# Optimization experiments

Hardware: AMD Instinct MI355X
Metric: run time of the kernel (lower is better)

The kernel has to match this reference:

```python
import jax, jax.numpy as jnp
import numpy as np

T_STEPS, N, STATE, HID, ACT, C = 32, 64, 64, 128, 32, 96


def setup_inputs() -> dict:
    key = jax.random.key(0)
    ks = jax.random.split(key, 16)
    s = 0.05
    inp = {
        'x': jax.random.normal(ks[0], (T_STEPS, N, STATE), jnp.float32),
        'a': jax.random.normal(ks[1], (T_STEPS, N, ACT), jnp.float32),
        # GRU layer 0 (input state_dim) and layer 1 (input hidden_dim)
        'wih0': jax.random.normal(ks[2], (3 * HID, STATE), jnp.float32) * s,
        'whh0': jax.random.normal(ks[3], (3 * HID, HID), jnp.float32) * s,
        'bih0': jax.random.normal(ks[4], (3 * HID,), jnp.float32) * s,
        'bhh0': jax.random.normal(ks[5], (3 * HID,), jnp.float32) * s,
        'wih1': jax.random.normal(ks[6], (3 * HID, HID), jnp.float32) * s,
        'whh1': jax.random.normal(ks[7], (3 * HID, HID), jnp.float32) * s,
        'bih1': jax.random.normal(ks[8], (3 * HID,), jnp.float32) * s,
        'bhh1': jax.random.normal(ks[9], (3 * HID,), jnp.float32) * s,
        'w1': jax.random.normal(ks[10], (HID, HID + ACT), jnp.float32) * s,
        'b1': jax.random.normal(ks[11], (HID,), jnp.float32) * s,
        'w2': jax.random.normal(ks[12], (1, 2 * HID), jnp.float32) * s,
        'b2': jax.random.normal(ks[13], (1,), jnp.float32) * s,
        'Tm': jax.random.normal(ks[14], (HID, HID, C), jnp.float32),  # init.normal(T,0,1)
    }
    return inp


def _gru_cell(x_t, h, wih, whh, bih, bhh):
    gi = x_t @ wih.T + bih            # (N, 3H)
    gh = h @ whh.T + bhh
    i_r, i_z, i_n = jnp.split(gi, 3, axis=-1)
    h_r, h_z, h_n = jnp.split(gh, 3, axis=-1)
    r = jax.nn.sigmoid(i_r + h_r)
    z = jax.nn.sigmoid(i_z + h_z)
    n = jnp.tanh(i_n + r * h_n)
    return (1.0 - z) * n + z * h


def reference(x, a, wih0, whh0, bih0, bhh0, wih1, whh1, bih1, bhh1, w1, b1, w2, b2, Tm):
    def step(h, x_t):
        h0 = _gru_cell(x_t, h[0], wih0, whh0, bih0, bhh0)
        h1 = _gru_cell(h0, h[1], wih1, whh1, bih1, bhh1)
        return jnp.stack([h0, h1]), h1

    h_init = jnp.zeros((2, N, HID), x.dtype)
    _, p = jax.lax.scan(step, h_init, x)              # (T, N, H)

    fc1 = jax.nn.relu(jnp.concatenate([p, a], -1) @ w1.T + b1)  # (T, N, H)

    Tflat = Tm.reshape(HID, HID * C)

    def batch_discrim(xt):  # xt: (N, H)
        M = (xt @ Tflat).reshape(N, HID, C)           # (N, B, C)
        # pairwise L1 over C: (N, N, B)
        norm = jnp.abs(M[:, None] - M[None, :]).sum(-1)
        o_b = (jnp.exp(-norm).sum(0) - 1.0) / (N - 1)  # (N, B)
        return jnp.concatenate([xt, o_b], 1)          # (N, 2H)

    fc2 = jax.lax.map(batch_discrim, fc1)             # (T, N, 2H)
    prob = jax.nn.sigmoid(fc2 @ w2.T + b2)            # (T, N, 1)
    return prob
```

## Files before the change

kernel.cpp:

```cpp
#include <hip/hip_runtime.h>
#include <hip/hip_fp16.h>
#include <cstdint>

#define T_STEPS 32
#define NB 64
#define STATE 64
#define HID 128
#define ACT 32
#define CDIM 96
#define G3 (3*HID)

typedef __attribute__((ext_vector_type(8))) short short8;
typedef __attribute__((ext_vector_type(4))) float f32x4;
typedef _Float16 h2v __attribute__((ext_vector_type(2)));

__device__ __forceinline__ unsigned short f2bf(float f){
  unsigned int u = __builtin_bit_cast(unsigned int, f);
  u = u + 0x7FFFu + ((u >> 16) & 1u);
  return (unsigned short)(u >> 16);
}
__device__ __forceinline__ float bf2f(unsigned short u){
  unsigned int v = ((unsigned int)u) << 16; return __builtin_bit_cast(float, v);
}
__device__ __forceinline__ unsigned int packh2(float f0, float f1){
  return (unsigned int)__half_as_ushort(__float2half_rn(f0)) |
         ((unsigned int)__half_as_ushort(__float2half_rn(f1)) << 16);
}
__device__ __forceinline__ float sigmoidf_(float x){ return 1.0f/(1.0f + __expf(-x)); }
__device__ __forceinline__ float tanhf_(float x){ float e = __expf(2.0f*x); return (e-1.0f)/(e+1.0f); }

__device__ __forceinline__ float dot2f(float acc, unsigned int a, unsigned int b){
  h2v av = __builtin_bit_cast(h2v, a);
  h2v bv = __builtin_bit_cast(h2v, b);
  return __builtin_amdgcn_fdot2(av, bv, acc, false);
}
__device__ __forceinline__ float l1d(float acc, unsigned int ua, unsigned int ub){
  __half2 a = __builtin_bit_cast(__half2, ua);
  __half2 b = __builtin_bit_cast(__half2, ub);
  __half2 d = __habs2(__hsub2(a, b));
  h2v dv = __builtin_bit_cast(h2v, d);
  h2v ones; ones[0] = (_Float16)1.0f; ones[1] = (_Float16)1.0f;
  return __builtin_amdgcn_fdot2(dv, ones, acc, false);
}
__device__ __forceinline__ float l1d4(float acc, uint4 a, uint4 b){
  acc = l1d(acc, a.x, b.x); acc = l1d(acc, a.y, b.y);
  acc = l1d(acc, a.z, b.z); acc = l1d(acc, a.w, b.w);
  return acc;
}

__global__ void k_prep(const float* __restrict__ Tm, unsigned short* __restrict__ tmh,
                       const float* __restrict__ whh0, const float* __restrict__ whh1,
                       const float* __restrict__ w1, const float* __restrict__ wih0,
                       const float* __restrict__ wih1, const float* __restrict__ x,
                       const float* __restrict__ a,
                       unsigned int* __restrict__ whh0p, unsigned int* __restrict__ whh1p,
                       unsigned short* __restrict__ w1f, unsigned short* __restrict__ wi0f,
                       unsigned short* __restrict__ wi1f, unsigned short* __restrict__ xaf,
                       unsigned short* __restrict__ h1af){
  __shared__ __align__(4) unsigned short lt[12800];
  int tid = threadIdx.x;
  int bx = blockIdx.x;
  if (bx < 128){
    int b = bx;
    unsigned int* l2 = (unsigned int*)lt;
    for (int e4 = tid; e4 < 3072; e4 += 256){
      int k = e4 / 24, c4 = (e4 - k*24)*4;
      const float4 v = *(const float4*)(Tm + k*(HID*CDIM) + b*CDIM + c4);
      int base = (k*100 + c4) >> 1;
      l2[base]   = (unsigned int)f2bf(v.x) | ((unsigned int)f2bf(v.y) << 16);
      l2[base+1] = (unsigned int)f2bf(v.z) | ((unsigned int)f2bf(v.w) << 16);
    }
    __syncthreads();
    unsigned int* tm2 = (unsigned int*)(tmh + b*(HID*CDIM));
    for (int e2 = tid; e2 < 6144; e2 += 256){
      int e = e2*2;
      int chunk = e / 768;
      int r1 = e - chunk*768;
      int c = r1 >> 3, h = r1 & 7;
      unsigned int lo = lt[(chunk*8 + h)*100 + c];
      unsigned int hi = lt[(chunk*8 + h + 1)*100 + c];
      tm2[e2] = lo | (hi << 16);
    }
  } else if (bx < 132){
    for (int e = (bx-128)*256 + tid; e < 24576; e += 1024){
      int k2 = e / 384, r = e - k2*384;
      whh0p[e] = packh2(whh0[r*128 + 2*k2], whh0[r*128 + 2*k2 + 1]);
      whh1p[e] = packh2(whh1[r*128 + 2*k2], whh1[r*128 + 2*k2 + 1]);
    }
  } else if (bx < 136){
    for (int e = (bx-132)*256 + tid; e < 20480; e += 1024){
      int kc = e >> 10, rem = e & 1023;
      int col = rem >> 3, j = rem & 7;
      w1f[e] = f2bf(w1[col*160 + kc*8 + j]);
    }
  } else if (bx < 140){
    for (int e = (bx-136)*256 + tid; e < 24576; e += 1024){
      int kc = e / 3072, rem = e - kc*3072;
      int col = rem >> 3, kl = rem & 7;
      wi0f[e] = f2bf(wih0[col*64 + kc*8 + kl]);
    }
  } else if (bx < 144){
    for (int e = (bx-140)*256 + tid; e < 49152; e += 1024){
      int kc = e / 3072, rem = e - kc*3072;
      int col = rem >> 3, kl = rem & 7;
      wi1f[e] = f2bf(wih1[col*128 + kc*8 + kl]);
    }
  } else if (bx < 156){
    for (int e = (bx-144)*256 + tid; e < 131072; e += 3072){
      int t = e >> 12, rem = e & 4095;
      int ntile = rem >> 10, rem2 = rem & 1023;
      int kc = rem2 >> 7, nl = (rem2 >> 3) & 15, kl = rem2 & 7;
      int n = ntile*16 + nl, k = kc*8 + kl;
      xaf[e] = f2bf(x[t*4096 + n*64 + k]);
    }
  } else {
    for (int e = (bx-156)*256 + tid; e < 65536; e += 3072){
      int t = e >> 11, rem = e & 2047;
      int n = rem >> 5, c = rem & 31;
      int pos = t*10240 + (n>>4)*2560 + (16 + (c>>3))*128 + (n&15)*8 + (c&7);
      h1af[pos] = f2bf(a[t*(NB*ACT) + n*ACT + c]);
    }
  }
}

template<int KK, int TSU>
__global__ __launch_bounds__(256) void k_gi(const unsigned short* __restrict__ af,
                                            const unsigned short* __restrict__ wf,
                                            const float* __restrict__ bias,
                                            float* __restrict__ gig){
  int t = blockIdx.x, by = blockIdx.y, tid = threadIdx.x;
  int wave = tid >> 6, lane = tid & 63, m = lane & 15, quad = lane >> 4;
  const uint4* A4 = (const uint4*)af;
  const uint4* B4 = (const uint4*)wf;
  uint4 av[KK];
  #pragma unroll
  for (int kk = 0; kk < KK; kk++) av[kk] = A4[t*TSU + wave*(TSU/4) + (kk*4+quad)*16 + m];
  f32x4 acc[6];
  #pragma unroll
  for (int i = 0; i < 6; i++) acc[i] = (f32x4)(0.0f);
  #pragma unroll
  for (int kk = 0; kk < KK; kk++){
    short8 a = __builtin_bit_cast(short8, av[kk]);
    #pragma unroll
    for (int ntl = 0; ntl < 6; ntl++){
      int nt = by*6 + ntl;
      uint4 bv = B4[(kk*4+quad)*384 + nt*16 + m];
      acc[ntl] = __builtin_amdgcn_mfma_f32_16x16x32_bf16(a, __builtin_bit_cast(short8, bv), acc[ntl], 0, 0, 0);
    }
  }
  #pragma unroll
  for (int ntl = 0; ntl < 6; ntl++){
    int col = (by*6+ntl)*16 + m;
    float bv = bias[col];
    #pragma unroll
    for (int rr = 0; rr < 4; rr++){
      int n = wave*16 + quad*4 + rr;
      gig[(t*NB + n)*G3 + col] = acc[ntl][rr] + bv;
    }
  }
}

template<int TS, int NS>
__global__ __launch_bounds__(768, 3) void k_rec(const unsigned int* __restrict__ whhp,
                                                const float* __restrict__ bhh,
                                                const float* __restrict__ gig,
                                                unsigned short* __restrict__ haf){
  __shared__ __align__(16) unsigned int hl[64];
  __shared__ float A0[G3];
  __shared__ __align__(16) float gl[T_STEPS*G3];
  __shared__ __align__(16) unsigned short hist[T_STEPS*HID];
  int n = blockIdx.x, tid = threadIdx.x;
  int r = tid >> 1, kh = tid & 1;
  {
    const float4* gg = (const float4*)gig;
    float4* gl4 = (float4*)gl;
    #pragma unroll
    for (int k = 0; k < 4; k++){
      int e = k*768 + tid;
      int t = e / 96, c = e - t*96;
      gl4[t*96 + c] = gg[(t*NB + n)*96 + c];
    }
  }
  unsigned int wh[32];
  #pragma unroll
  for (int i = 0; i < 32; i++) wh[i] = whhp[(kh*32 + i)*384 + r];
  float bh = (kh == 0) ? bhh[r] : 0.0f;
  if (tid < 64) hl[tid] = 0u;
  float hprev = 0.0f;
  __syncthreads();
  const uint4* h4 = (const uint4*)hl;
  for (int t = 0; t < T_STEPS; t++){
    float s0 = 0.0f, s1 = 0.0f, s2 = 0.0f, s3 = 0.0f;
    #pragma unroll
    for (int g = 0; g < 2; g++){
      uint4 hv[4];
      #pragma unroll
      for (int j = 0; j < 4; j++) hv[j] = h4[kh*8 + g*4 + j];
      s0 = dot2f(s0, wh[g*16 + 0], hv[0].x);  s0 = dot2f(s0, wh[g*16 + 1], hv[0].y);
      s0 = dot2f(s0, wh[g*16 + 2], hv[0].z);  s0 = dot2f(s0, wh[g*16 + 3], hv[0].w);
      s1 = dot2f(s1, wh[g*16 + 4], hv[1].x);  s1 = dot2f(s1, wh[g*16 + 5], hv[1].y);
      s1 = dot2f(s1, wh[g*16 + 6], hv[1].z);  s1 = dot2f(s1, wh[g*16 + 7], hv[1].w);
      s2 = dot2f(s2, wh[g*16 + 8], hv[2].x);  s2 = dot2f(s2, wh[g*16 + 9], hv[2].y);
      s2 = dot2f(s2, wh[g*16 +10], hv[2].z);  s2 = dot2f(s2, wh[g*16 +11], hv[2].w);
      s3 = dot2f(s3, wh[g*16 +12], hv[3].x);  s3 = dot2f(s3, wh[g*16 +13], hv[3].y);
      s3 = dot2f(s3, wh[g*16 +14], hv[3].z);  s3 = dot2f(s3, wh[g*16 +15], hv[3].w);
    }
    float gh = bh + ((s0 + s1) + (s2 + s3));
    gh += __shfl_xor(gh, 1);
    if (kh == 0) A0[r] = gh;
    __syncthreads();
    if (tid < HID){
      const float* gp = gl + t*G3;
      float rg = sigmoidf_(gp[tid]       + A0[tid]);
      float z  = sigmoidf_(gp[tid+HID]   + A0[tid+HID]);
      float nn = tanhf_   (gp[tid+2*HID] + rg*A0[tid+2*HID]);
      float hn = (1.0f - z)*nn + z*hprev;
      hprev = hn;
      ((__half*)hl)[tid] = __float2half_rn(hn);
      hist[t*HID + tid] = f2bf(hn);
    }
    __syncthreads();
  }
  if (tid < T_STEPS*16){
    int t = tid >> 4, j = tid & 15;
    uint4 v = *(const uint4*)(hist + t*HID + j*8);
    *(uint4*)(haf + t*TS + (n>>4)*NS + j*128 + (n&15)*8) = v;
  }
}

__global__ __launch_bounds__(256) void k_fc1(const unsigned short* __restrict__ h1af,
                                             const unsigned short* __restrict__ w1f,
                                             const float* __restrict__ b1,
                                             unsigned short* __restrict__ fc1h){
  __shared__ float b1s[128];
  int t = blockIdx.x, tid = threadIdx.x;
  int wave = tid >> 6, lane = tid & 63, m = lane & 15, quad = lane >> 4;
  if (tid < 128) b1s[tid] = b1[tid];
  const uint4* A4 = (const uint4*)(h1af + t*10240);
  const uint4* B4 = (const uint4*)w1f;
  f32x4 acc[8];
  #pragma unroll
  for (int i = 0; i < 8; i++) acc[i] = (f32x4)(0.0f);
  #pragma unroll
  for (int ks = 0; ks < 5; ks++){
    uint4 av = A4[wave*320 + (ks*4 + quad)*16 + m];
    short8 avs = __builtin_bit_cast(short8, av);
    #pragma unroll
    for (int nt = 0; nt < 8; nt++){
      uint4 bv = B4[(ks*4 + quad)*128 + nt*16 + m];
      acc[nt] = __builtin_amdgcn_mfma_f32_16x16x32_bf16(avs, __builtin_bit_cast(short8, bv), acc[nt], 0, 0, 0);
    }
  }
  __syncthreads();
  #pragma unroll
  for (int nt = 0; nt < 8; nt++){
    float bj = b1s[nt*16 + m];
    #pragma unroll
    for (int rr = 0; rr < 4; rr++){
      float v = fmaxf(acc[nt][rr] + bj, 0.0f);
      fc1h[t*8192 + wave*2048 + (nt*2 + (m>>3))*128 + (quad*4 + rr)*8 + (m&7)] = f2bf(v);
    }
  }
}

__global__ __launch_bounds__(256) void k_disc(const unsigned short* __restrict__ fc1h,
                                              const unsigned short* __restrict__ tmh,
                                              float* __restrict__ O){
  __shared__ __align__(16) __half Mh[64*120];
  __shared__ unsigned short plist[2016];
  __shared__ float osum[64];
  __shared__ unsigned int cnt;
  int b = blockIdx.x, t = blockIdx.y;
  int tid = threadIdx.x;
  int wave = tid >> 6, lane = tid & 63, m = lane & 15, quad = lane >> 4;
  if (tid < 64) osum[tid] = 0.0f;
  if (tid == 0) cnt = 0u;
  const uint4* Bg = (const uint4*)(tmh + b*(CDIM*HID));
  const uint4* Ag = (const uint4*)(fc1h + t*8192);
  uint4 a4[4];
  #pragma unroll
  for (int kk = 0; kk < 4; kk++) a4[kk] = Ag[wave*256 + (kk*4 + quad)*16 + m];
  f32x4 acc[6];
  #pragma unroll
  for (int i = 0; i < 6; i++) acc[i] = (f32x4)(0.0f);
  #pragma unroll
  for (int kk = 0; kk < 4; kk++){
    short8 av = __builtin_bit_cast(short8, a4[kk]);
    #pragma unroll
    for (int nt = 0; nt < 6; nt++){
      uint4 b4 = Bg[(kk*4 + quad)*96 + nt*16 + m];
      acc[nt] = __builtin_amdgcn_mfma_f32_16x16x32_bf16(av, __builtin_bit_cast(short8, b4), acc[nt], 0, 0, 0);
    }
  }
  #pragma unroll
  for (int nt = 0; nt < 6; nt++){
    #pragma unroll
    for (int rr = 0; rr < 4; rr++){
      Mh[(wave*16 + quad*4 + rr)*120 + nt*16 + m] = __float2half(acc[nt][rr]);
    }
  }
  __syncthreads();
  const unsigned int ONES2 = 0x3C003C00u;
  #pragma unroll
  for (int idx = tid; idx < 512; idx += 256){
    int r = idx >> 3, jc = idx & 7;
    const unsigned int* row = (const unsigned int*)(Mh + r*120 + jc*12);
    float s = 0.0f;
    #pragma unroll
    for (int q = 0; q < 6; q++) s = dot2f(s, row[q], ONES2);
    Mh[r*120 + 96 + jc] = __float2half(s);
  }
  __syncthreads();
  const uint4* M4 = (const uint4*)Mh;
  for (int p = tid; p < 2016; p += 256){
    int r = p >> 5, s = p & 31;
    int i, j;
    if (s == 0){ i = 63; j = r; }
    else {
      i = r + s;      if (i >= 63) i -= 63;
      j = r + 63 - s; if (j >= 63) j -= 63;
    }
    uint4 qa = M4[i*15 + 12];
    uint4 qb = M4[j*15 + 12];
    float lb = l1d4(0.0f, qa, qb);
    if (lb <= 14.5f){
      unsigned int k = atomicAdd(&cnt, 1u);
      plist[k] = (unsigned short)(i*64 + j);
    }
  }
  __syncthreads();
  int ns = (int)cnt;
  if (ns > 2016) ns = 2016;
  for (int v = tid; v < ns; v += 256){
    int pr = plist[v];
    int i = pr >> 6, j = pr & 63;
    float L = 0.0f;
    #pragma unroll
    for (int c = 0; c < 12; c++){
      L = l1d4(L, M4[i*15 + c], M4[j*15 + c]);
    }
    float e = __expf(-L);
    atomicAdd(&osum[i], e);
    atomicAdd(&osum[j], e);
  }
  __syncthreads();
  if (tid < 64) O[(t*HID + b)*NB + tid] = osum[tid]*(1.0f/63.0f);
}

__global__ __launch_bounds__(256) void k_final(const unsigned short* __restrict__ fc1h,
                                               const float* __restrict__ O,
                                               const float* __restrict__ w2, const float* __restrict__ b2,
                                               float* __restrict__ out){
  __shared__ float ol[NB*HID];
  __shared__ unsigned short fr[8192];
  __shared__ float wl[2*HID + 2];
  __shared__ float pp[4][NB];
  int t = blockIdx.x, tid = threadIdx.x;
  for (int i = tid; i < NB*HID; i += 256) ol[i] = O[t*NB*HID + i];
  const uint4* Fg = (const uint4*)(fc1h + t*8192);
  for (int i = tid; i < 1024; i += 256) ((uint4*)fr)[i] = Fg[i];
  if (tid < 2*HID) wl[tid] = w2[tid];
  if (tid == 0) wl[2*HID] = b2[0];
  __syncthreads();
  int n = tid & 63, part = tid >> 6;
  float acc = 0.0f;
  int base = (n>>4)*2048 + (n&15)*8;
  #pragma unroll
  for (int jc = 0; jc < 4; jc++){
    int j8 = part*4 + jc;
    #pragma unroll
    for (int k = 0; k < 8; k++)
      acc += bf2f(fr[base + j8*128 + k])*wl[j8*8 + k];
  }
  #pragma unroll 8
  for (int bb = 0; bb < 32; bb++){
    int bq = part*32 + bb;
    acc += ol[bq*NB + n]*wl[HID + bq];
  }
  pp[part][n] = acc;
  __syncthreads();
  if (tid < NB){
    float s = wl[2*HID] + pp[0][tid] + pp[1][tid] + pp[2][tid] + pp[3][tid];
    out[t*NB + tid] = sigmoidf_(s);
  }
}

extern "C" void kernel_launch(void* const* d_in, const int* in_sizes, int n_in,
                              void* d_out, int out_size, void* d_ws, size_t ws_size,
                              hipStream_t stream){
  const float* x    = (const float*)d_in[0];
  const float* a    = (const float*)d_in[1];
  const float* wih0 = (const float*)d_in[2];
  const float* whh0 = (const float*)d_in[3];
  const float* bih0 = (const float*)d_in[4];
  const float* bhh0 = (const float*)d_in[5];
  const float* wih1 = (const float*)d_in[6];
  const float* whh1 = (const float*)d_in[7];
  const float* bih1 = (const float*)d_in[8];
  const float* bhh1 = (const float*)d_in[9];
  const float* w1   = (const float*)d_in[10];
  const float* b1   = (const float*)d_in[11];
  const float* w2   = (const float*)d_in[12];
  const float* b2   = (const float*)d_in[13];
  const float* Tm   = (const float*)d_in[14];
  float* ws = (float*)d_ws;
  float* Ows = ws;
  unsigned int* whh0p = (unsigned int*)(ws + 262144);
  unsigned int* whh1p = (unsigned int*)(ws + 286720);
  unsigned short* tmh  = (unsigned short*)(ws + 311296);
  unsigned short* fc1h = (unsigned short*)(ws + 1097728);
  unsigned short* h1af = (unsigned short*)(ws + 1228800);
  unsigned short* w1f  = (unsigned short*)(ws + 1392640);
  unsigned short* xaf  = (unsigned short*)(ws + 1402880);
  unsigned short* wi0f = (unsigned short*)(ws + 1468416);
  unsigned short* wi1f = (unsigned short*)(ws + 1480704);
  unsigned short* h0af = (unsigned short*)(ws + 1505280);
  float* gig = ws + 1636352;
  float* out = (float*)d_out;

  k_prep<<<dim3(168), dim3(256), 0, stream>>>(Tm, tmh, whh0, whh1, w1, wih0, wih1, x, a,
                                              whh0p, whh1p, w1f, wi0f, wi1f, xaf, h1af);
  k_gi<2, 512><<<dim3(T_STEPS, 4), dim3(256), 0, stream>>>(xaf, wi0f, bih0, gig);
  k_rec<8192, 2048><<<dim3(NB), dim3(768), 0, stream>>>(whh0p, bhh0, gig, h0af);
  k_gi<4, 1024><<<dim3(T_STEPS, 4), dim3(256), 0, stream>>>(h0af, wi1f, bih1, gig);
  k_rec<10240, 2560><<<dim3(NB), dim3(768), 0, stream>>>(whh1p, bhh1, gig, h1af);
  k_fc1<<<dim3(T_STEPS), dim3(256), 0, stream>>>(h1af, w1f, b1, fc1h);
  k_disc<<<dim3(HID, T_STEPS), dim3(256), 0, stream>>>(fc1h, tmh, Ows);
  k_final<<<dim3(T_STEPS), dim3(256), 0, stream>>>(fc1h, Ows, w2, b2, out);
}
```

Before: 184.4 us.

## Fuse both GRU layers into one recurrent kernel with in-loop layer-1 input projection

Merges the two recurrent kernels and the layer-1 input-projection GEMM into a single kernel. Each step computes layer 0, then layer 1's input gates from the fresh h0 using fp16-packed wih1 held in registers, then the layer-1 update. This removes two launches and the h0 and gig round trips through global memory. In exchange, each step in the serial loop does more dot-product work and has more barriers, and per-thread register use triples (96 weight registers), which may limit occupancy.

Result: no change. 186.7 us (+1.2%).

```diff
diff --git a/kernel.cpp b/kernel.cpp
--- a/kernel.cpp
+++ b/kernel.cpp
@@ -55,7 +55,7 @@
                        const float* __restrict__ a,
                        unsigned int* __restrict__ whh0p, unsigned int* __restrict__ whh1p,
                        unsigned short* __restrict__ w1f, unsigned short* __restrict__ wi0f,
-                       unsigned short* __restrict__ wi1f, unsigned short* __restrict__ xaf,
+                       unsigned int* __restrict__ wi1p, unsigned short* __restrict__ xaf,
                        unsigned short* __restrict__ h1af){
   __shared__ __align__(4) unsigned short lt[12800];
   int tid = threadIdx.x;
@@ -100,10 +100,9 @@
       wi0f[e] = f2bf(wih0[col*64 + kc*8 + kl]);
     }
   } else if (bx < 144){
-    for (int e = (bx-140)*256 + tid; e < 49152; e += 1024){
-      int kc = e / 3072, rem = e - kc*3072;
-      int col = rem >> 3, kl = rem & 7;
-      wi1f[e] = f2bf(wih1[col*128 + kc*8 + kl]);
+    for (int e = (bx-140)*256 + tid; e < 24576; e += 1024){
+      int k2 = e / 384, r = e - k2*384;
+      wi1p[e] = packh2(wih1[r*128 + 2*k2], wih1[r*128 + 2*k2 + 1]);
     }
   } else if (bx < 156){
     for (int e = (bx-144)*256 + tid; e < 131072; e += 3072){
@@ -160,13 +159,19 @@
   }
 }
 
-template<int TS, int NS>
-__global__ __launch_bounds__(768, 3) void k_rec(const unsigned int* __restrict__ whhp,
-                                                const float* __restrict__ bhh,
-                                                const float* __restrict__ gig,
-                                                unsigned short* __restrict__ haf){
-  __shared__ __align__(16) unsigned int hl[64];
+__global__ __launch_bounds__(768, 3) void k_rec2(const unsigned int* __restrict__ whh0p,
+                                                 const unsigned int* __restrict__ whh1p,
+                                                 const unsigned int* __restrict__ wi1p,
+                                                 const float* __restrict__ bhh0,
+                                                 const float* __restrict__ bhh1,
+                                                 const float* __restrict__ bih1,
+                                                 const float* __restrict__ gig,
+                                                 unsigned short* __restrict__ h1af){
+  __shared__ __align__(16) unsigned int h0l[64];
+  __shared__ __align__(16) unsigned int h1l[64];
   __shared__ float A0[G3];
+  __shared__ float AH[G3];
+  __shared__ float AI[G3];
   __shared__ __align__(16) float gl[T_STEPS*G3];
   __shared__ __align__(16) unsigned short hist[T_STEPS*HID];
   int n = blockIdx.x, tid = threadIdx.x;
@@ -181,42 +186,88 @@
       gl4[t*96 + c] = gg[(t*NB + n)*96 + c];
     }
   }
-  unsigned int wh[32];
-  #pragma unroll
-  for (int i = 0; i < 32; i++) wh[i] = whhp[(kh*32 + i)*384 + r];
-  float bh = (kh == 0) ? bhh[r] : 0.0f;
-  if (tid < 64) hl[tid] = 0u;
-  float hprev = 0.0f;
-  __syncthreads();
-  const uint4* h4 = (const uint4*)hl;
+  unsigned int wh0[32], wh1[32], wi1[32];
+  #pragma unroll
+  for (int i = 0; i < 32; i++){
+    wh0[i] = whh0p[(kh*32 + i)*384 + r];
+    wh1[i] = whh1p[(kh*32 + i)*384 + r];
+    wi1[i] = wi1p [(kh*32 + i)*384 + r];
+  }
+  float bh0 = (kh == 0) ? bhh0[r] : 0.0f;
+  float bh1 = (kh == 0) ? bhh1[r] : 0.0f;
+  float bi1 = (kh == 0) ? bih1[r] : 0.0f;
+  if (tid < 64){ h0l[tid] = 0u; h1l[tid] = 0u; }
+  float h0prev = 0.0f, h1prev = 0.0f;
+  __syncthreads();
+  const uint4* h40 = (const uint4*)h0l;
+  const uint4* h41 = (const uint4*)h1l;
   for (int t = 0; t < T_STEPS; t++){
     float s0 = 0.0f, s1 = 0.0f, s2 = 0.0f, s3 = 0.0f;
+    float u0 = 0.0f, u1 = 0.0f, u2 = 0.0f, u3 = 0.0f;
     #pragma unroll
     for (int g = 0; g < 2; g++){
-      uint4 hv[4];
-      #pragma unroll
-      for (int j = 0; j < 4; j++) hv[j] = h4[kh*8 + g*4 + j];
-      s0 = dot2f(s0, wh[g*16 + 0], hv[0].x);  s0 = dot2f(s0, wh[g*16 + 1], hv[0].y);
-      s0 = dot2f(s0, wh[g*16 + 2], hv[0].z);  s0 = dot2f(s0, wh[g*16 + 3], hv[0].w);
-      s1 = dot2f(s1, wh[g*16 + 4], hv[1].x);  s1 = dot2f(s1, wh[g*16 + 5], hv[1].y);
-      s1 = dot2f(s1, wh[g*16 + 6], hv[1].z);  s1 = dot2f(s1, wh[g*16 + 7], hv[1].w);
-      s2 = dot2f(s2, wh[g*16 + 8], hv[2].x);  s2 = dot2f(s2, wh[g*16 + 9], hv[2].y);
-      s2 = dot2f(s2, wh[g*16 +10], hv[2].z);  s2 = dot2f(s2, wh[g*16 +11], hv[2].w);
-      s3 = dot2f(s3, wh[g*16 +12], hv[3].x);  s3 = dot2f(s3, wh[g*16 +13], hv[3].y);
-      s3 = dot2f(s3, wh[g*16 +14], hv[3].z);  s3 = dot2f(s3, wh[g*16 +15], hv[3].w);
-    }
-    float gh = bh + ((s0 + s1) + (s2 + s3));
-    gh += __shfl_xor(gh, 1);
-    if (kh == 0) A0[r] = gh;
+      uint4 a0 = h40[kh*8 + g*4 + 0], a1 = h40[kh*8 + g*4 + 1];
+      uint4 a2 = h40[kh*8 + g*4 + 2], a3 = h40[kh*8 + g*4 + 3];
+      uint4 b0 = h41[kh*8 + g*4 + 0], b1 = h41[kh*8 + g*4 + 1];
+      uint4 b2 = h41[kh*8 + g*4 + 2], b3 = h41[kh*8 + g*4 + 3];
+      s0 = dot2f(s0, wh0[g*16 + 0], a0.x);  s0 = dot2f(s0, wh0[g*16 + 1], a0.y);
+      s0 = dot2f(s0, wh0[g*16 + 2], a0.z);  s0 = dot2f(s0, wh0[g*16 + 3], a0.w);
+      s1 = dot2f(s1, wh0[g*16 + 4], a1.x);  s1 = dot2f(s1, wh0[g*16 + 5], a1.y);
+      s1 = dot2f(s1, wh0[g*16 + 6], a1.z);  s1 = dot2f(s1, wh0[g*16 + 7], a1.w);
+      s2 = dot2f(s2, wh0[g*16 + 8], a2.x);  s2 = dot2f(s2, wh0[g*16 + 9], a2.y);
+      s2 = dot2f(s2, wh0[g*16 +10], a2.z);  s2 = dot2f(s2, wh0[g*16 +11], a2.w);
+      s3 = dot2f(s3, wh0[g*16 +12], a3.x);  s3 = dot2f(s3, wh0[g*16 +13], a3.y);
+      s3 = dot2f(s3, wh0[g*16 +14], a3.z);  s3 = dot2f(s3, wh0[g*16 +15], a3.w);
+      u0 = dot2f(u0, wh1[g*16 + 0], b0.x);  u0 = dot2f(u0, wh1[g*16 + 1], b0.y);
+      u0 = dot2f(u0, wh1[g*16 + 2], b0.z);  u0 = dot2f(u0, wh1[g*16 + 3], b0.w);
+      u1 = dot2f(u1, wh1[g*16 + 4], b1.x);  u1 = dot2f(u1, wh1[g*16 + 5], b1.y);
+      u1 = dot2f(u1, wh1[g*16 + 6], b1.z);  u1 = dot2f(u1, wh1[g*16 + 7], b1.w);
+      u2 = dot2f(u2, wh1[g*16 + 8], b2.x);  u2 = dot2f(u2, wh1[g*16 + 9], b2.y);
+      u2 = dot2f(u2, wh1[g*16 +10], b2.z);  u2 = dot2f(u2, wh1[g*16 +11], b2.w);
+      u3 = dot2f(u3, wh1[g*16 +12], b3.x);  u3 = dot2f(u3, wh1[g*16 +13], b3.y);
+      u3 = dot2f(u3, wh1[g*16 +14], b3.z);  u3 = dot2f(u3, wh1[g*16 +15], b3.w);
+    }
+    float gh0 = bh0 + ((s0 + s1) + (s2 + s3));
+    float gh1 = bh1 + ((u0 + u1) + (u2 + u3));
+    gh0 += __shfl_xor(gh0, 1);
+    gh1 += __shfl_xor(gh1, 1);
+    if (kh == 0){ A0[r] = gh0; AH[r] = gh1; }
     __syncthreads();
     if (tid < HID){
       const float* gp = gl + t*G3;
       float rg = sigmoidf_(gp[tid]       + A0[tid]);
       float z  = sigmoidf_(gp[tid+HID]   + A0[tid+HID]);
       float nn = tanhf_   (gp[tid+2*HID] + rg*A0[tid+2*HID]);
-      float hn = (1.0f - z)*nn + z*hprev;
-      hprev = hn;
-      ((__half*)hl)[tid] = __float2half_rn(hn);
+      float hn = (1.0f - z)*nn + z*h0prev;
+      h0prev = hn;
+      ((__half*)h0l)[tid] = __float2half_rn(hn);
+    }
+    __syncthreads();
+    float q0 = 0.0f, q1 = 0.0f, q2 = 0.0f, q3 = 0.0f;
+    #pragma unroll
+    for (int g = 0; g < 2; g++){
+      uint4 a0 = h40[kh*8 + g*4 + 0], a1 = h40[kh*8 + g*4 + 1];
+      uint4 a2 = h40[kh*8 + g*4 + 2], a3 = h40[kh*8 + g*4 + 3];
+      q0 = dot2f(q0, wi1[g*16 + 0], a0.x);  q0 = dot2f(q0, wi1[g*16 + 1], a0.y);
+      q0 = dot2f(q0, wi1[g*16 + 2], a0.z);  q0 = dot2f(q0, wi1[g*16 + 3], a0.w);
+      q1 = dot2f(q1, wi1[g*16 + 4], a1.x);  q1 = dot2f(q1, wi1[g*16 + 5], a1.y);
+      q1 = dot2f(q1, wi1[g*16 + 6], a1.z);  q1 = dot2f(q1, wi1[g*16 + 7], a1.w);
+      q2 = dot2f(q2, wi1[g*16 + 8], a2.x);  q2 = dot2f(q2, wi1[g*16 + 9], a2.y);
+      q2 = dot2f(q2, wi1[g*16 +10], a2.z);  q2 = dot2f(q2, wi1[g*16 +11], a2.w);
+      q3 = dot2f(q3, wi1[g*16 +12], a3.x);  q3 = dot2f(q3, wi1[g*16 +13], a3.y);
+      q3 = dot2f(q3, wi1[g*16 +14], a3.z);  q3 = dot2f(q3, wi1[g*16 +15], a3.w);
+    }
+    float gi = bi1 + ((q0 + q1) + (q2 + q3));
+    gi += __shfl_xor(gi, 1);
+    if (kh == 0) AI[r] = gi;
+    __syncthreads();
+    if (tid < HID){
+      float rg = sigmoidf_(AI[tid]       + AH[tid]);
+      float z  = sigmoidf_(AI[tid+HID]   + AH[tid+HID]);
+      float nn = tanhf_   (AI[tid+2*HID] + rg*AH[tid+2*HID]);
+      float hn = (1.0f - z)*nn + z*h1prev;
+      h1prev = hn;
+      ((__half*)h1l)[tid] = __float2half_rn(hn);
       hist[t*HID + tid] = f2bf(hn);
     }
     __syncthreads();
@@ -224,7 +275,7 @@
   if (tid < T_STEPS*16){
     int t = tid >> 4, j = tid & 15;
     uint4 v = *(const uint4*)(hist + t*HID + j*8);
-    *(uint4*)(haf + t*TS + (n>>4)*NS + j*128 + (n&15)*8) = v;
+    *(uint4*)(h1af + t*10240 + (n>>4)*2560 + j*128 + (n&15)*8) = v;
   }
 }
 
@@ -413,17 +464,14 @@
   unsigned short* w1f  = (unsigned short*)(ws + 1392640);
   unsigned short* xaf  = (unsigned short*)(ws + 1402880);
   unsigned short* wi0f = (unsigned short*)(ws + 1468416);
-  unsigned short* wi1f = (unsigned short*)(ws + 1480704);
-  unsigned short* h0af = (unsigned short*)(ws + 1505280);
+  unsigned int*   wi1p = (unsigned int*)(ws + 1480704);
   float* gig = ws + 1636352;
   float* out = (float*)d_out;
 
   k_prep<<<dim3(168), dim3(256), 0, stream>>>(Tm, tmh, whh0, whh1, w1, wih0, wih1, x, a,
-                                              whh0p, whh1p, w1f, wi0f, wi1f, xaf, h1af);
+                                              whh0p, whh1p, w1f, wi0f, wi1p, xaf, h1af);
   k_gi<2, 512><<<dim3(T_STEPS, 4), dim3(256), 0, stream>>>(xaf, wi0f, bih0, gig);
-  k_rec<8192, 2048><<<dim3(NB), dim3(768), 0, stream>>>(whh0p, bhh0, gig, h0af);
-  k_gi<4, 1024><<<dim3(T_STEPS, 4), dim3(256), 0, stream>>>(h0af, wi1f, bih1, gig);
-  k_rec<10240, 2560><<<dim3(NB), dim3(768), 0, stream>>>(whh1p, bhh1, gig, h1af);
+  k_rec2<<<dim3(NB), dim3(768), 0, stream>>>(whh0p, whh1p, wi1p, bhh0, bhh1, bih1, gig, h1af);
   k_fc1<<<dim3(T_STEPS), dim3(256), 0, stream>>>(h1af, w1f, b1, fc1h);
   k_disc<<<dim3(HID, T_STEPS), dim3(256), 0, stream>>>(fc1h, tmh, Ows);
   k_final<<<dim3(T_STEPS), dim3(256), 0, stream>>>(fc1h, Ows, w2, b2, out);
```

## Fuse both GRU layer recurrences and layer-1 input projection into one kernel

Applied to the files above, without the earlier changes.

Replaces the three launches (layer-0 recurrence, layer-1 input GEMM, layer-1 recurrence) with a single per-sequence kernel. After layer 0, each block keeps its hidden history in padded LDS and computes the layer-1 input gates with MFMA straight into shared memory, then runs the layer-1 recurrence. This removes two launches and the global round trips for h0 and the layer-1 gate buffer. In exchange, the per-block GEMM runs on only 64 blocks and LDS use per block grows, which may reduce occupancy.

New measurement: 180.4 us, median of 2. 1.02x faster.

```diff
diff --git a/kernel.cpp b/kernel.cpp
--- a/kernel.cpp
+++ b/kernel.cpp
@@ -160,15 +160,19 @@
   }
 }
 
-template<int TS, int NS>
-__global__ __launch_bounds__(768, 3) void k_rec(const unsigned int* __restrict__ whhp,
-                                                const float* __restrict__ bhh,
-                                                const float* __restrict__ gig,
-                                                unsigned short* __restrict__ haf){
+__global__ __launch_bounds__(768, 3) void k_rec2(const unsigned int* __restrict__ whh0p,
+                                                 const unsigned int* __restrict__ whh1p,
+                                                 const float* __restrict__ bhh0,
+                                                 const float* __restrict__ bhh1,
+                                                 const float* __restrict__ bih1,
+                                                 const unsigned short* __restrict__ wi1f,
+                                                 const float* __restrict__ gig,
+                                                 unsigned short* __restrict__ h1af){
   __shared__ __align__(16) unsigned int hl[64];
   __shared__ float A0[G3];
   __shared__ __align__(16) float gl[T_STEPS*G3];
-  __shared__ __align__(16) unsigned short hist[T_STEPS*HID];
+  __shared__ __align__(16) unsigned short hist0[T_STEPS*136];
+  __shared__ __align__(16) unsigned short hist1[T_STEPS*HID];
   int n = blockIdx.x, tid = threadIdx.x;
   int r = tid >> 1, kh = tid & 1;
   {
@@ -183,8 +187,8 @@
   }
   unsigned int wh[32];
   #pragma unroll
-  for (int i = 0; i < 32; i++) wh[i] = whhp[(kh*32 + i)*384 + r];
-  float bh = (kh == 0) ? bhh[r] : 0.0f;
+  for (int i = 0; i < 32; i++) wh[i] = whh0p[(kh*32 + i)*384 + r];
+  float bh = (kh == 0) ? bhh0[r] : 0.0f;
   if (tid < 64) hl[tid] = 0u;
   float hprev = 0.0f;
   __syncthreads();
@@ -217,14 +221,85 @@
       float hn = (1.0f - z)*nn + z*hprev;
       hprev = hn;
       ((__half*)hl)[tid] = __float2half_rn(hn);
-      hist[t*HID + tid] = f2bf(hn);
+      hist0[t*136 + tid] = f2bf(hn);
+    }
+    __syncthreads();
+  }
+  {
+    int wave = tid >> 6, lane = tid & 63, m = lane & 15, quad = lane >> 4;
+    const uint4* B4 = (const uint4*)wi1f;
+    const uint4* H4 = (const uint4*)hist0;
+    f32x4 acc00 = (f32x4)(0.0f), acc01 = (f32x4)(0.0f);
+    f32x4 acc10 = (f32x4)(0.0f), acc11 = (f32x4)(0.0f);
+    int nt0 = wave*2;
+    #pragma unroll
+    for (int kk = 0; kk < 4; kk++){
+      uint4 a0 = H4[m*17 + kk*4 + quad];
+      uint4 a1 = H4[(16 + m)*17 + kk*4 + quad];
+      uint4 b0 = B4[(kk*4 + quad)*384 + nt0*16 + m];
+      uint4 b1 = B4[(kk*4 + quad)*384 + (nt0+1)*16 + m];
+      short8 a0s = __builtin_bit_cast(short8, a0);
+      short8 a1s = __builtin_bit_cast(short8, a1);
+      short8 b0s = __builtin_bit_cast(short8, b0);
+      short8 b1s = __builtin_bit_cast(short8, b1);
+      acc00 = __builtin_amdgcn_mfma_f32_16x16x32_bf16(a0s, b0s, acc00, 0, 0, 0);
+      acc01 = __builtin_amdgcn_mfma_f32_16x16x32_bf16(a0s, b1s, acc01, 0, 0, 0);
+      acc10 = __builtin_amdgcn_mfma_f32_16x16x32_bf16(a1s, b0s, acc10, 0, 0, 0);
+      acc11 = __builtin_amdgcn_mfma_f32_16x16x32_bf16(a1s, b1s, acc11, 0, 0, 0);
+    }
+    float bv0 = bih1[nt0*16 + m];
+    float bv1 = bih1[(nt0+1)*16 + m];
+    #pragma unroll
+    for (int rr = 0; rr < 4; rr++){
+      gl[(quad*4 + rr)*G3 + nt0*16 + m]        = acc00[rr] + bv0;
+      gl[(quad*4 + rr)*G3 + (nt0+1)*16 + m]    = acc01[rr] + bv1;
+      gl[(16 + quad*4 + rr)*G3 + nt0*16 + m]   = acc10[rr] + bv0;
+      gl[(16 + quad*4 + rr)*G3 + (nt0+1)*16 + m] = acc11[rr] + bv1;
+    }
+  }
+  asm volatile("" ::: "memory");
+  #pragma unroll
+  for (int i = 0; i < 32; i++) wh[i] = whh1p[(kh*32 + i)*384 + r];
+  bh = (kh == 0) ? bhh1[r] : 0.0f;
+  if (tid < 64) hl[tid] = 0u;
+  hprev = 0.0f;
+  __syncthreads();
+  for (int t = 0; t < T_STEPS; t++){
+    float s0 = 0.0f, s1 = 0.0f, s2 = 0.0f, s3 = 0.0f;
+    #pragma unroll
+    for (int g = 0; g < 2; g++){
+      uint4 hv[4];
+      #pragma unroll
+      for (int j = 0; j < 4; j++) hv[j] = h4[kh*8 + g*4 + j];
+      s0 = dot2f(s0, wh[g*16 + 0], hv[0].x);  s0 = dot2f(s0, wh[g*16 + 1], hv[0].y);
+      s0 = dot2f(s0, wh[g*16 + 2], hv[0].z);  s0 = dot2f(s0, wh[g*16 + 3], hv[0].w);
+      s1 = dot2f(s1, wh[g*16 + 4], hv[1].x);  s1 = dot2f(s1, wh[g*16 + 5], hv[1].y);
+      s1 = dot2f(s1, wh[g*16 + 6], hv[1].z);  s1 = dot2f(s1, wh[g*16 + 7], hv[1].w);
+      s2 = dot2f(s2, wh[g*16 + 8], hv[2].x);  s2 = dot2f(s2, wh[g*16 + 9], hv[2].y);
+      s2 = dot2f(s2, wh[g*16 +10], hv[2].z);  s2 = dot2f(s2, wh[g*16 +11], hv[2].w);
+      s3 = dot2f(s3, wh[g*16 +12], hv[3].x);  s3 = dot2f(s3, wh[g*16 +13], hv[3].y);
+      s3 = dot2f(s3, wh[g*16 +14], hv[3].z);  s3 = dot2f(s3, wh[g*16 +15], hv[3].w);
+    }
+    float gh = bh + ((s0 + s1) + (s2 + s3));
+    gh += __shfl_xor(gh, 1);
+    if (kh == 0) A0[r] = gh;
+    __syncthreads();
+    if (tid < HID){
+      const float* gp = gl + t*G3;
+      float rg = sigmoidf_(gp[tid]       + A0[tid]);
+      float z  = sigmoidf_(gp[tid+HID]   + A0[tid+HID]);
+      float nn = tanhf_   (gp[tid+2*HID] + rg*A0[tid+2*HID]);
+      float hn = (1.0f - z)*nn + z*hprev;
+      hprev = hn;
+      ((__half*)hl)[tid] = __float2half_rn(hn);
+      hist1[t*HID + tid] = f2bf(hn);
     }
     __syncthreads();
   }
   if (tid < T_STEPS*16){
     int t = tid >> 4, j = tid & 15;
-    uint4 v = *(const uint4*)(hist + t*HID + j*8);
-    *(uint4*)(haf + t*TS + (n>>4)*NS + j*128 + (n&15)*8) = v;
+    uint4 v = *(const uint4*)(hist1 + t*HID + j*8);
+    *(uint4*)(h1af + t*10240 + (n>>4)*2560 + j*128 + (n&15)*8) = v;
   }
 }
 
@@ -414,16 +489,13 @@
   unsigned short* xaf  = (unsigned short*)(ws + 1402880);
   unsigned short* wi0f = (unsigned short*)(ws + 1468416);
   unsigned short* wi1f = (unsigned short*)(ws + 1480704);
-  unsigned short* h0af = (unsigned short*)(ws + 1505280);
   float* gig = ws + 1636352;
   float* out = (float*)d_out;
 
   k_prep<<<dim3(168), dim3(256), 0, stream>>>(Tm, tmh, whh0, whh1, w1, wih0, wih1, x, a,
                                               whh0p, whh1p, w1f, wi0f, wi1f, xaf, h1af);
   k_gi<2, 512><<<dim3(T_STEPS, 4), dim3(256), 0, stream>>>(xaf, wi0f, bih0, gig);
-  k_rec<8192, 2048><<<dim3(NB), dim3(768), 0, stream>>>(whh0p, bhh0, gig, h0af);
-  k_gi<4, 1024><<<dim3(T_STEPS, 4), dim3(256), 0, stream>>>(h0af, wi1f, bih1, gig);
-  k_rec<10240, 2560><<<dim3(NB), dim3(768), 0, stream>>>(whh1p, bhh1, gig, h1af);
+  k_rec2<<<dim3(NB), dim3(768), 0, stream>>>(whh0p, whh1p, bhh0, bhh1, bih1, wi1f, gig, h1af);
   k_fc1<<<dim3(T_STEPS), dim3(256), 0, stream>>>(h1af, w1f, b1, fc1h);
   k_disc<<<dim3(HID, T_STEPS), dim3(256), 0, stream>>>(fc1h, tmh, Ows);
   k_final<<<dim3(T_STEPS), dim3(256), 0, stream>>>(fc1h, Ows, w2, b2, out);
```
